# Kernel optimization log

Hardware: AMD Instinct MI355X
Metric: run time of the kernel (lower is better)

Reference implementation:

```python
import jax, jax.numpy as jnp
import numpy as np

B, L, H, V = 16, 512, 256, 32000
HALF = H // 2
EPS_LN = 1e-5
EPS_NORM = 1e-12


def setup_inputs() -> dict:
    key = jax.random.key(0)
    ks = jax.random.split(key, 9)
    s = 0.02
    return {
        "seq": jax.random.randint(ks[0], (B, L), 0, V),
        "embed": jax.random.normal(ks[1], (V, H), jnp.float32) * s,
        "W1": jax.random.normal(ks[2], (2 * H, H), jnp.float32) * s,
        "b1": jnp.zeros((2 * H,), jnp.float32),
        "W2": jax.random.normal(ks[3], (H, 2 * H), jnp.float32) * s,
        "b2": jnp.zeros((H,), jnp.float32),
        "gamma": jnp.ones((H,), jnp.float32),
        "beta": jnp.zeros((H,), jnp.float32),
        "W_sem": jax.random.normal(ks[4], (HALF, H), jnp.float32) * s,
        "W_epi": jax.random.normal(ks[5], (HALF, H), jnp.float32) * s,
        "W_rp": jax.random.normal(ks[6], (H, H), jnp.float32) * s,
        "b_rp": jnp.zeros((H,), jnp.float32),
        "W_out": jax.random.normal(ks[7], (V, H), jnp.float32) * s,
        "b_out": jnp.zeros((V,), jnp.float32),
    }


def _l2norm(x):
    # F.normalize(dim=-1): x / max(||x||, eps)
    n = jnp.sqrt(jnp.sum(x * x, axis=-1, keepdims=True))
    return x / jnp.maximum(n, EPS_NORM)


def reference(seq, embed, W1, b1, W2, b2, gamma, beta, W_sem, W_epi, W_rp, b_rp, W_out, b_out):
    h = embed[seq]                                   # [B, L, H]
    ff = jnp.maximum(h @ W1.T + b1, 0.0) @ W2.T + b2  # MLP with 2H hidden
    x = h + ff
    mu = jnp.mean(x, axis=-1, keepdims=True)
    var = jnp.var(x, axis=-1, keepdims=True)
    h = (x - mu) / jnp.sqrt(var + EPS_LN) * gamma + beta  # LayerNorm

    ks_all = jnp.einsum('blh,kh->blk', h, W_sem)     # [B, L, HALF]
    ke_all = jnp.einsum('blh,kh->blk', h, W_epi)

    def step(carry, kv):
        M_s, M_e = carry
        k_s, k_e = kv                                 # [B, HALF] each
        kns = _l2norm(k_s)
        kne = _l2norm(k_e)
        vps = jnp.einsum('bij,bj->bi', M_s, kns)      # read from fast weights
        vpe = jnp.einsum('bij,bj->bi', M_e, kne)
        M_s = M_s + jnp.einsum('bi,bj->bij', k_s - vps, kns)  # delta-rule write
        M_e = M_e + jnp.einsum('bi,bj->bij', k_e - vpe, kne)
        return (M_s, M_e), None

    M0 = jnp.zeros((B, HALF, HALF), h.dtype)
    # scan over timesteps 0..L-2 (time-major)
    (M_s, M_e), _ = jax.lax.scan(
        step, (M0, M0),
        (jnp.swapaxes(ks_all[:, :-1], 0, 1), jnp.swapaxes(ke_all[:, :-1], 0, 1)))

    cs = jnp.einsum('bij,bj->bi', M_s, ks_all[:, -1])  # read with last-token query
    ce = jnp.einsum('bij,bj->bi', M_e, ke_all[:, -1])
    c = jnp.concatenate([cs, ce], axis=-1)             # [B, H]
    r = c @ W_rp.T + b_rp
    return r @ W_out.T + b_out                          # [B, V]
```

## Files before the change

kernel.cpp:

```cpp
#include <hip/hip_runtime.h>

#define B_ 16
#define L_ 512
#define H_ 256
#define V_ 32000
#define HALF_ 128

typedef __attribute__((ext_vector_type(8))) short short8;
typedef __attribute__((ext_vector_type(4))) float floatx4;

__device__ __forceinline__ unsigned short f2bf(float x) {
  unsigned int u = __float_as_uint(x);
  unsigned int r = (u + 0x7FFFu + ((u >> 16) & 1u)) >> 16;
  return (unsigned short)r;
}

#define BL_(u) __uint_as_float((u) << 16)
#define BH_(u) __uint_as_float((u) & 0xffff0000u)

template <int CTRL>
__device__ __forceinline__ float dpp_xor_add(float x) {
  int y = __builtin_amdgcn_mov_dpp(__float_as_int(x), CTRL, 0xf, 0xf, true);
  return x + __int_as_float(y);
}

__device__ __forceinline__ float redu16(float p) {
  p = dpp_xor_add<0xB1>(p);
  p = dpp_xor_add<0x4E>(p);
  p = dpp_xor_add<0x141>(p);
  p = dpp_xor_add<0x140>(p);
  return p;
}

__global__ __launch_bounds__(256) void prep_kernel(const int* __restrict__ seq,
                                                   const float* __restrict__ embed,
                                                   float* __restrict__ h,
                                                   unsigned short* __restrict__ hbf,
                                                   const float* __restrict__ W1,
                                                   const float* __restrict__ W2,
                                                   const float* __restrict__ Ws,
                                                   const float* __restrict__ We,
                                                   unsigned short* __restrict__ W1b,
                                                   unsigned short* __restrict__ W2b,
                                                   unsigned short* __restrict__ Wcb) {
  int blk = blockIdx.x;
  int tid = threadIdx.x;
  if (blk < 2048) {
    int token = blk * 4 + (tid >> 6);
    int lane = tid & 63;
    int row = seq[token];
    float4 v = ((const float4*)(embed + (size_t)row * H_))[lane];
    ((float4*)(h + (size_t)token * H_))[lane] = v;
    ushort4 o;
    o.x = f2bf(v.x); o.y = f2bf(v.y); o.z = f2bf(v.z); o.w = f2bf(v.w);
    *(ushort4*)(hbf + (size_t)token * H_ + lane * 4) = o;
  } else {
    int i = (blk - 2048) * 256 + tid;
    if (i < 131072) W1b[i] = f2bf(W1[i]);
    else if (i < 262144) W2b[i - 131072] = f2bf(W2[i - 131072]);
    else if (i < 294912) Wcb[i - 262144] = f2bf(Ws[i - 262144]);
    else Wcb[i - 262144] = f2bf(We[i - 294912]);
  }
}

template <int MT, bool RELU, bool BIAS, bool RES, bool OUT_BF16>
__global__ __launch_bounds__(256) void gemm_mfma(const unsigned short* __restrict__ A,
                                                 const unsigned short* __restrict__ Bw,
                                                 const float* __restrict__ bias,
                                                 const float* __restrict__ Res,
                                                 float* __restrict__ Cf,
                                                 unsigned short* __restrict__ Cb,
                                                 int M, int N, int K) {
  constexpr int FI = MT / 32;
  __shared__ unsigned short As[MT * 40];
  __shared__ unsigned short Bs[128 * 40];
  int tid = threadIdx.x;
  int wave = tid >> 6, lane = tid & 63;
  int wm = (wave >> 1) * (MT / 2), wn = (wave & 1) * 64;
  int quad = lane >> 4, l15 = lane & 15;
  int bm = blockIdx.y * MT, bn = blockIdx.x * 128;
  int sr = tid >> 2, sq = tid & 3;

  floatx4 zero = {0.f, 0.f, 0.f, 0.f};
  floatx4 acc[FI][4];
#pragma unroll
  for (int fi = 0; fi < FI; fi++)
#pragma unroll
    for (int fj = 0; fj < 4; fj++) acc[fi][fj] = zero;

  for (int k0 = 0; k0 < K; k0 += 32) {
    uint4 av0 = *(const uint4*)(A + (size_t)(bm + sr) * K + k0 + sq * 8);
    uint4 av1;
    if (MT == 128) av1 = *(const uint4*)(A + (size_t)(bm + 64 + sr) * K + k0 + sq * 8);
    uint4 bv0 = *(const uint4*)(Bw + (size_t)(bn + sr) * K + k0 + sq * 8);
    uint4 bv1 = *(const uint4*)(Bw + (size_t)(bn + 64 + sr) * K + k0 + sq * 8);
    __syncthreads();
    *(uint4*)(As + sr * 40 + sq * 8) = av0;
    if (MT == 128) *(uint4*)(As + (64 + sr) * 40 + sq * 8) = av1;
    *(uint4*)(Bs + sr * 40 + sq * 8) = bv0;
    *(uint4*)(Bs + (64 + sr) * 40 + sq * 8) = bv1;
    __syncthreads();
    short8 af[FI], bf[4];
#pragma unroll
    for (int f = 0; f < FI; f++) af[f] = *(const short8*)(As + (wm + f * 16 + l15) * 40 + quad * 8);
#pragma unroll
    for (int f = 0; f < 4; f++) bf[f] = *(const short8*)(Bs + (wn + f * 16 + l15) * 40 + quad * 8);
#pragma unroll
    for (int fi = 0; fi < FI; fi++)
#pragma unroll
      for (int fj = 0; fj < 4; fj++)
        acc[fi][fj] = __builtin_amdgcn_mfma_f32_16x16x32_bf16(af[fi], bf[fj], acc[fi][fj], 0, 0, 0);
  }

#pragma unroll
  for (int fi = 0; fi < FI; fi++) {
#pragma unroll
    for (int fj = 0; fj < 4; fj++) {
      int col = bn + wn + fj * 16 + l15;
      float bb = BIAS ? bias[col] : 0.f;
#pragma unroll
      for (int rg = 0; rg < 4; rg++) {
        int row = bm + wm + fi * 16 + quad * 4 + rg;
        float v = acc[fi][fj][rg] + bb;
        if (RES) v += Res[(size_t)row * N + col];
        if (RELU) v = fmaxf(v, 0.f);
        if (OUT_BF16) Cb[(size_t)row * N + col] = f2bf(v);
        else Cf[(size_t)row * N + col] = v;
      }
    }
  }
}

__global__ void ln_kernel(const float* __restrict__ x, const float* __restrict__ gamma,
                          const float* __restrict__ beta, unsigned short* __restrict__ yb) {
  int row = blockIdx.x;
  int lane = threadIdx.x;
  float4 v = ((const float4*)(x + (size_t)row * H_))[lane];
  float s = v.x + v.y + v.z + v.w;
  float sq = v.x * v.x + v.y * v.y + v.z * v.z + v.w * v.w;
#pragma unroll
  for (int off = 32; off >= 1; off >>= 1) {
    s += __shfl_xor(s, off);
    sq += __shfl_xor(sq, off);
  }
  float mu = s * (1.f / H_);
  float var = sq * (1.f / H_) - mu * mu;
  float inv = rsqrtf(var + 1e-5f);
  float4 g = ((const float4*)gamma)[lane];
  float4 b = ((const float4*)beta)[lane];
  ushort4 o;
  o.x = f2bf((v.x - mu) * inv * g.x + b.x);
  o.y = f2bf((v.y - mu) * inv * g.y + b.y);
  o.z = f2bf((v.z - mu) * inv * g.z + b.z);
  o.w = f2bf((v.w - mu) * inv * g.w + b.w);
  *(ushort4*)(yb + (size_t)row * H_ + lane * 4) = o;
}

__global__ __launch_bounds__(256) void normalize_kernel(const float* __restrict__ kcat,
                                                        unsigned short* __restrict__ khat) {
  int e = blockIdx.x * 4 + (threadIdx.x >> 6);
  int lane = threadIdx.x & 63;
  int idxm = e >> 9, t = e & 511;
  int b = idxm >> 1, mat = idxm & 1;
  const float* kp = kcat + ((size_t)b * L_ + t) * 256 + mat * 128;
  float2 v = ((const float2*)kp)[lane];
  float s = v.x * v.x + v.y * v.y;
#pragma unroll
  for (int off = 32; off >= 1; off >>= 1) s += __shfl_xor(s, off);
  float inv = 1.f / fmaxf(sqrtf(s), 1e-12f);
  ushort2 o;
  o.x = f2bf(v.x * inv);
  o.y = f2bf(v.y * inv);
  *(ushort2*)(khat + (size_t)e * HALF_ + lane * 2) = o;
}

__global__ __launch_bounds__(256) void gram_kernel(const unsigned short* __restrict__ khat,
                                                   float* __restrict__ gram) {
  int e = blockIdx.x * 4 + (threadIdx.x >> 6);
  int lane = threadIdx.x & 63;
  int idxm = e >> 7, ch = e & 127;
  const unsigned short* kp = khat + ((size_t)idxm * L_ + ch * 4) * HALF_ + lane * 2;
  float2 a[4];
#pragma unroll
  for (int i = 0; i < 4; i++) {
    unsigned int w = *(const unsigned int*)(kp + i * HALF_);
    a[i].x = BL_(w);
    a[i].y = BH_(w);
  }
  float s01 = a[0].x * a[1].x + a[0].y * a[1].y;
  float s02 = a[0].x * a[2].x + a[0].y * a[2].y;
  float s03 = a[0].x * a[3].x + a[0].y * a[3].y;
  float s12 = a[1].x * a[2].x + a[1].y * a[2].y;
  float s13 = a[1].x * a[3].x + a[1].y * a[3].y;
  float s23 = a[2].x * a[3].x + a[2].y * a[3].y;
#pragma unroll
  for (int off = 32; off >= 1; off >>= 1) {
    s01 += __shfl_xor(s01, off);
    s02 += __shfl_xor(s02, off);
    s03 += __shfl_xor(s03, off);
    s12 += __shfl_xor(s12, off);
    s13 += __shfl_xor(s13, off);
    s23 += __shfl_xor(s23, off);
  }
  if (lane == 0) {
    float4 g0 = {s01, s02, s03, s12};
    float2 g1 = {s13, s23};
    *(float4*)(gram + (size_t)e * 8) = g0;
    *(float2*)(gram + (size_t)e * 8 + 4) = g1;
  }
}

#define UNPK(P, K)                                                         \
  float K##0 = BL_(P.x), K##1 = BH_(P.x), K##2 = BL_(P.y), K##3 = BH_(P.y), \
        K##4 = BL_(P.z), K##5 = BH_(P.z), K##6 = BL_(P.w), K##7 = BH_(P.w);

#define DOT8(K, OUT)                                                     \
  float OUT;                                                             \
  {                                                                      \
    float a_ = m[0] * K##0 + m[1] * K##1, b_ = m[2] * K##2 + m[3] * K##3, \
          c_ = m[4] * K##4 + m[5] * K##5, d_ = m[6] * K##6 + m[7] * K##7; \
    OUT = (a_ + b_) + (c_ + d_);                                         \
  }

#define SCAN_STEP(PK, PR)                                                \
  do {                                                                   \
    UNPK(PK, kz)                                                         \
    DOT8(kz, p_)                                                         \
    p_ = redu16(p_);                                                     \
    float sS = PR - p_;                                                  \
    m[0] += sS * kz0; m[1] += sS * kz1; m[2] += sS * kz2; m[3] += sS * kz3; \
    m[4] += sS * kz4; m[5] += sS * kz5; m[6] += sS * kz6; m[7] += sS * kz7; \
  } while (0)

__global__ __launch_bounds__(256) void scan_kernel(const float* __restrict__ kcat,
                                                   const unsigned short* __restrict__ khat,
                                                   const float* __restrict__ gram,
                                                   float* __restrict__ c) {
  int bid = blockIdx.x;
  int idxm = bid & 31;
  int rg = bid >> 5;
  int b = idxm >> 1, mat = idxm & 1;
  const unsigned short* kh = khat + (size_t)idxm * L_ * HALF_;
  const float* kbase = kcat + (size_t)b * L_ * 256 + mat * HALF_;
  const float* gp = gram + (size_t)idxm * 128 * 8;

  int tid = threadIdx.x;
  int seg = tid & 15;
  int rl = tid >> 4;
  int r = rg * 16 + rl;
  int c0 = seg * 8;
  const float* krow = kbase + r;

  float m[8];
#pragma unroll
  for (int g = 0; g < 8; g++) m[g] = 0.f;

  uint4 pk0 = *(const uint4*)(kh + 0 * HALF_ + c0);
  uint4 pk1 = *(const uint4*)(kh + 1 * HALF_ + c0);
  uint4 pk2 = *(const uint4*)(kh + 2 * HALF_ + c0);
  uint4 pk3 = *(const uint4*)(kh + 3 * HALF_ + c0);
  float pr0 = krow[0], pr1 = krow[256], pr2 = krow[512], pr3 = krow[768];
  float4 g03 = *(const float4*)(gp);
  float2 g45 = *(const float2*)(gp + 4);

  for (int ch = 0; ch < 127; ch++) {
    const unsigned short* kn = kh + (size_t)(ch + 1) * 4 * HALF_ + c0;
    uint4 n0 = *(const uint4*)(kn);
    uint4 n1 = *(const uint4*)(kn + HALF_);
    uint4 n2 = *(const uint4*)(kn + 2 * HALF_);
    uint4 n3 = *(const uint4*)(kn + 3 * HALF_);
    const float* rn = krow + (size_t)(ch + 1) * 4 * 256;
    float nr0 = rn[0], nr1 = rn[256], nr2 = rn[512], nr3 = rn[768];
    float4 ng03 = *(const float4*)(gp + (size_t)(ch + 1) * 8);
    float2 ng45 = *(const float2*)(gp + (size_t)(ch + 1) * 8 + 4);

    {
      UNPK(pk0, ka) UNPK(pk1, kb) UNPK(pk2, kc) UNPK(pk3, kd)
      DOT8(ka, p0) DOT8(kb, p1) DOT8(kc, p2) DOT8(kd, p3)
      p0 = redu16(p0);
      p1 = redu16(p1);
      p2 = redu16(p2);
      p3 = redu16(p3);
      float d0 = pr0 - p0;
      float d1 = pr1 - p1 - g03.x * d0;
      float d2 = pr2 - p2 - g03.y * d0 - g03.w * d1;
      float d3 = pr3 - p3 - g03.z * d0 - g45.x * d1 - g45.y * d2;
      m[0] += d0 * ka0 + d1 * kb0 + d2 * kc0 + d3 * kd0;
      m[1] += d0 * ka1 + d1 * kb1 + d2 * kc1 + d3 * kd1;
      m[2] += d0 * ka2 + d1 * kb2 + d2 * kc2 + d3 * kd2;
      m[3] += d0 * ka3 + d1 * kb3 + d2 * kc3 + d3 * kd3;
      m[4] += d0 * ka4 + d1 * kb4 + d2 * kc4 + d3 * kd4;
      m[5] += d0 * ka5 + d1 * kb5 + d2 * kc5 + d3 * kd5;
      m[6] += d0 * ka6 + d1 * kb6 + d2 * kc6 + d3 * kd6;
      m[7] += d0 * ka7 + d1 * kb7 + d2 * kc7 + d3 * kd7;
    }

    pk0 = n0; pk1 = n1; pk2 = n2; pk3 = n3;
    pr0 = nr0; pr1 = nr1; pr2 = nr2; pr3 = nr3;
    g03 = ng03; g45 = ng45;
  }

  SCAN_STEP(pk0, pr0);
  SCAN_STEP(pk1, pr1);
  SCAN_STEP(pk2, pr2);

  float4 qa = *(const float4*)(kbase + (size_t)511 * 256 + c0);
  float4 qb = *(const float4*)(kbase + (size_t)511 * 256 + c0 + 4);
  float pa = m[0] * qa.x + m[1] * qa.y, pb2 = m[2] * qa.z + m[3] * qa.w;
  float pc = m[4] * qb.x + m[5] * qb.y, pd = m[6] * qb.z + m[7] * qb.w;
  float p = redu16((pa + pb2) + (pc + pd));
  if (seg == 0) c[(size_t)b * H_ + mat * HALF_ + r] = p;
}

__global__ void rp_kernel(const float* __restrict__ c, const float* __restrict__ Wrp,
                          const float* __restrict__ brp, float* __restrict__ r) {
  int b = blockIdx.x;
  int n = threadIdx.x;
  __shared__ float cs[H_];
  cs[n] = c[(size_t)b * H_ + n];
  __syncthreads();
  const float4* w4 = (const float4*)(Wrp + (size_t)n * H_);
  const float4* c4 = (const float4*)cs;
  float acc = 0.f;
#pragma unroll 8
  for (int k = 0; k < H_ / 4; k++) {
    float4 w = w4[k], cc = c4[k];
    acc += w.x * cc.x + w.y * cc.y + w.z * cc.z + w.w * cc.w;
  }
  r[(size_t)b * H_ + n] = acc + brp[n];
}

__global__ __launch_bounds__(256) void out_kernel(const float* __restrict__ r,
                                                  const float* __restrict__ Wout,
                                                  const float* __restrict__ bout,
                                                  float* __restrict__ out) {
  __shared__ float rs[16 * 272];
  __shared__ float obuf[16 * 68];
  int tid = threadIdx.x;
#pragma unroll
  for (int q = 0; q < 16; q++) {
    int idx = q * 256 + tid;
    int bb = idx >> 8, cc = idx & 255;
    rs[bb * 272 + cc + 4 * (cc >> 6)] = r[idx];
  }
  __syncthreads();
  int row = tid >> 2, part = tid & 3;
  int v = blockIdx.x * 64 + row;
  const float4* w4 = (const float4*)(Wout + (size_t)v * H_ + part * 64);
  float acc[16];
#pragma unroll
  for (int bb = 0; bb < 16; bb++) acc[bb] = 0.f;
#pragma unroll 4
  for (int j = 0; j < 16; j++) {
    float4 w = w4[j];
#pragma unroll
    for (int bb = 0; bb < 16; bb++) {
      float4 rv = *(const float4*)&rs[bb * 272 + part * 68 + j * 4];
      acc[bb] += w.x * rv.x + w.y * rv.y + w.z * rv.z + w.w * rv.w;
    }
  }
  float bo = bout[v];
#pragma unroll
  for (int bb = 0; bb < 16; bb++) {
    acc[bb] = dpp_xor_add<0xB1>(acc[bb]);
    acc[bb] = dpp_xor_add<0x4E>(acc[bb]);
  }
#pragma unroll
  for (int q = 0; q < 4; q++) {
    int bb = part * 4 + q;
    obuf[bb * 68 + row] = acc[bb] + bo;
  }
  __syncthreads();
#pragma unroll
  for (int q = 0; q < 4; q++) {
    int idx = q * 256 + tid;
    int bb = idx >> 6, vl = idx & 63;
    out[(size_t)bb * V_ + blockIdx.x * 64 + vl] = obuf[bb * 68 + vl];
  }
}

extern "C" void kernel_launch(void* const* d_in, const int* in_sizes, int n_in,
                              void* d_out, int out_size, void* d_ws, size_t ws_size,
                              hipStream_t stream) {
  const int* seq = (const int*)d_in[0];
  const float* embed = (const float*)d_in[1];
  const float* W1 = (const float*)d_in[2];
  const float* b1 = (const float*)d_in[3];
  const float* W2 = (const float*)d_in[4];
  const float* b2 = (const float*)d_in[5];
  const float* gamma = (const float*)d_in[6];
  const float* beta = (const float*)d_in[7];
  const float* Wsem = (const float*)d_in[8];
  const float* Wepi = (const float*)d_in[9];
  const float* Wrp = (const float*)d_in[10];
  const float* brp = (const float*)d_in[11];
  const float* Wout = (const float*)d_in[12];
  const float* bout = (const float*)d_in[13];
  float* out = (float*)d_out;

  float* ws = (float*)d_ws;
  float* h = ws;
  float* x = h;
  float* kcat = ws + 2097152;
  unsigned short* a1b = (unsigned short*)kcat;
  unsigned short* hbf = (unsigned short*)(ws + 4194304);
  float* gram = ws + 4718592;
  unsigned short* hnb = (unsigned short*)(ws + 5242880);
  unsigned short* khat = (unsigned short*)(ws + 6291456);
  unsigned short* W1b = (unsigned short*)(ws + 7340032);
  unsigned short* W2b = (unsigned short*)(ws + 7405568);
  unsigned short* Wcb = (unsigned short*)(ws + 7471104);
  float* c = ws + 7503872;
  float* r = ws + 7508000;

  prep_kernel<<<3328, 256, 0, stream>>>(seq, embed, h, hbf, W1, W2, Wsem, Wepi, W1b, W2b, Wcb);
  gemm_mfma<128, true, true, false, true><<<dim3(4, 64), 256, 0, stream>>>(
      hbf, W1b, b1, nullptr, nullptr, a1b, 8192, 512, 256);
  gemm_mfma<64, false, true, true, false><<<dim3(2, 128), 256, 0, stream>>>(
      a1b, W2b, b2, h, x, nullptr, 8192, 256, 512);
  ln_kernel<<<8192, 64, 0, stream>>>(x, gamma, beta, hnb);
  gemm_mfma<64, false, false, false, false><<<dim3(2, 128), 256, 0, stream>>>(
      hnb, Wcb, nullptr, nullptr, kcat, nullptr, 8192, 256, 256);
  normalize_kernel<<<4096, 256, 0, stream>>>(kcat, khat);
  gram_kernel<<<1024, 256, 0, stream>>>(khat, gram);
  scan_kernel<<<256, 256, 0, stream>>>(kcat, khat, gram, c);
  rp_kernel<<<16, 256, 0, stream>>>(c, Wrp, brp, r);
  out_kernel<<<500, 256, 0, stream>>>(r, Wout, bout, out);
}
```

Before: 271.7 us.

## Fuse key projection with L2 normalization and restructure scan with LDS-staged fp32 keys

Replaces the generic key-projection GEMM, normalize and Gram kernels with one kproj kernel. It computes both key projections per 32-row tile, L2-normalizes them in registers and writes fp32 normalized keys plus a transposed raw-key layout. The scan kernel drops the 4-step blocked Gram correction and instead runs the plain sequential delta rule, streaming normalized keys through double-buffered LDS filled by async global-to-LDS copies. The GEMM also gains register prefetch of the next K-slice, and the workspace layout is compacted. This removes two launches and intermediate round trips, but the scan now has a serial reduction on every step instead of one per four steps.

```diff
diff --git a/kernel.cpp b/kernel.cpp
--- a/kernel.cpp
+++ b/kernel.cpp
@@ -14,9 +14,6 @@
   unsigned int r = (u + 0x7FFFu + ((u >> 16) & 1u)) >> 16;
   return (unsigned short)r;
 }
-
-#define BL_(u) __uint_as_float((u) << 16)
-#define BH_(u) __uint_as_float((u) & 0xffff0000u)
 
 template <int CTRL>
 __device__ __forceinline__ float dpp_xor_add(float x) {
@@ -30,6 +27,12 @@
   p = dpp_xor_add<0x141>(p);
   p = dpp_xor_add<0x140>(p);
   return p;
+}
+
+__device__ __forceinline__ void async_cp16(const float* g, float* l) {
+  __builtin_amdgcn_global_load_lds(
+      (const __attribute__((address_space(1))) void*)g,
+      (__attribute__((address_space(3))) void*)l, 16, 0, 0);
 }
 
 __global__ __launch_bounds__(256) void prep_kernel(const int* __restrict__ seq,
@@ -88,18 +91,25 @@
 #pragma unroll
     for (int fj = 0; fj < 4; fj++) acc[fi][fj] = zero;
 
+  uint4 av0, av1, bv0, bv1;
+  av0 = *(const uint4*)(A + (size_t)(bm + sr) * K + sq * 8);
+  if (MT == 128) av1 = *(const uint4*)(A + (size_t)(bm + 64 + sr) * K + sq * 8);
+  bv0 = *(const uint4*)(Bw + (size_t)(bn + sr) * K + sq * 8);
+  bv1 = *(const uint4*)(Bw + (size_t)(bn + 64 + sr) * K + sq * 8);
+
   for (int k0 = 0; k0 < K; k0 += 32) {
-    uint4 av0 = *(const uint4*)(A + (size_t)(bm + sr) * K + k0 + sq * 8);
-    uint4 av1;
-    if (MT == 128) av1 = *(const uint4*)(A + (size_t)(bm + 64 + sr) * K + k0 + sq * 8);
-    uint4 bv0 = *(const uint4*)(Bw + (size_t)(bn + sr) * K + k0 + sq * 8);
-    uint4 bv1 = *(const uint4*)(Bw + (size_t)(bn + 64 + sr) * K + k0 + sq * 8);
     __syncthreads();
     *(uint4*)(As + sr * 40 + sq * 8) = av0;
     if (MT == 128) *(uint4*)(As + (64 + sr) * 40 + sq * 8) = av1;
     *(uint4*)(Bs + sr * 40 + sq * 8) = bv0;
     *(uint4*)(Bs + (64 + sr) * 40 + sq * 8) = bv1;
     __syncthreads();
+    if (k0 + 32 < K) {
+      av0 = *(const uint4*)(A + (size_t)(bm + sr) * K + k0 + 32 + sq * 8);
+      if (MT == 128) av1 = *(const uint4*)(A + (size_t)(bm + 64 + sr) * K + k0 + 32 + sq * 8);
+      bv0 = *(const uint4*)(Bw + (size_t)(bn + sr) * K + k0 + 32 + sq * 8);
+      bv1 = *(const uint4*)(Bw + (size_t)(bn + 64 + sr) * K + k0 + 32 + sq * 8);
+    }
     short8 af[FI], bf[4];
 #pragma unroll
     for (int f = 0; f < FI; f++) af[f] = *(const short8*)(As + (wm + f * 16 + l15) * 40 + quad * 8);
@@ -156,159 +166,201 @@
   *(ushort4*)(yb + (size_t)row * H_ + lane * 4) = o;
 }
 
-__global__ __launch_bounds__(256) void normalize_kernel(const float* __restrict__ kcat,
-                                                        unsigned short* __restrict__ khat) {
-  int e = blockIdx.x * 4 + (threadIdx.x >> 6);
-  int lane = threadIdx.x & 63;
-  int idxm = e >> 9, t = e & 511;
-  int b = idxm >> 1, mat = idxm & 1;
-  const float* kp = kcat + ((size_t)b * L_ + t) * 256 + mat * 128;
-  float2 v = ((const float2*)kp)[lane];
-  float s = v.x * v.x + v.y * v.y;
-#pragma unroll
-  for (int off = 32; off >= 1; off >>= 1) s += __shfl_xor(s, off);
-  float inv = 1.f / fmaxf(sqrtf(s), 1e-12f);
-  ushort2 o;
-  o.x = f2bf(v.x * inv);
-  o.y = f2bf(v.y * inv);
-  *(ushort2*)(khat + (size_t)e * HALF_ + lane * 2) = o;
-}
-
-__global__ __launch_bounds__(256) void gram_kernel(const unsigned short* __restrict__ khat,
-                                                   float* __restrict__ gram) {
-  int e = blockIdx.x * 4 + (threadIdx.x >> 6);
-  int lane = threadIdx.x & 63;
-  int idxm = e >> 7, ch = e & 127;
-  const unsigned short* kp = khat + ((size_t)idxm * L_ + ch * 4) * HALF_ + lane * 2;
-  float2 a[4];
-#pragma unroll
-  for (int i = 0; i < 4; i++) {
-    unsigned int w = *(const unsigned int*)(kp + i * HALF_);
-    a[i].x = BL_(w);
-    a[i].y = BH_(w);
-  }
-  float s01 = a[0].x * a[1].x + a[0].y * a[1].y;
-  float s02 = a[0].x * a[2].x + a[0].y * a[2].y;
-  float s03 = a[0].x * a[3].x + a[0].y * a[3].y;
-  float s12 = a[1].x * a[2].x + a[1].y * a[2].y;
-  float s13 = a[1].x * a[3].x + a[1].y * a[3].y;
-  float s23 = a[2].x * a[3].x + a[2].y * a[3].y;
-#pragma unroll
-  for (int off = 32; off >= 1; off >>= 1) {
-    s01 += __shfl_xor(s01, off);
-    s02 += __shfl_xor(s02, off);
-    s03 += __shfl_xor(s03, off);
-    s12 += __shfl_xor(s12, off);
-    s13 += __shfl_xor(s13, off);
-    s23 += __shfl_xor(s23, off);
-  }
-  if (lane == 0) {
-    float4 g0 = {s01, s02, s03, s12};
-    float2 g1 = {s13, s23};
-    *(float4*)(gram + (size_t)e * 8) = g0;
-    *(float2*)(gram + (size_t)e * 8 + 4) = g1;
-  }
-}
-
-#define UNPK(P, K)                                                         \
-  float K##0 = BL_(P.x), K##1 = BH_(P.x), K##2 = BL_(P.y), K##3 = BH_(P.y), \
-        K##4 = BL_(P.z), K##5 = BH_(P.z), K##6 = BL_(P.w), K##7 = BH_(P.w);
-
-#define DOT8(K, OUT)                                                     \
-  float OUT;                                                             \
-  {                                                                      \
-    float a_ = m[0] * K##0 + m[1] * K##1, b_ = m[2] * K##2 + m[3] * K##3, \
-          c_ = m[4] * K##4 + m[5] * K##5, d_ = m[6] * K##6 + m[7] * K##7; \
-    OUT = (a_ + b_) + (c_ + d_);                                         \
-  }
-
-#define SCAN_STEP(PK, PR)                                                \
+__global__ __launch_bounds__(256) void kproj_kernel(const unsigned short* __restrict__ hnb,
+                                                    const unsigned short* __restrict__ Wcb,
+                                                    float* __restrict__ khat,
+                                                    float* __restrict__ kT) {
+  __shared__ unsigned short As[32 * 40];
+  __shared__ unsigned short Bs[256 * 40];
+  int tid = threadIdx.x;
+  int wave = tid >> 6, lane = tid & 63;
+  int wm = (wave >> 1) * 16, wnh = wave & 1, wn = wnh * 128;
+  int quad = lane >> 4, l15 = lane & 15;
+  int bm = blockIdx.x * 32;
+
+  floatx4 zero = {0.f, 0.f, 0.f, 0.f};
+  floatx4 acc[8];
+#pragma unroll
+  for (int fj = 0; fj < 8; fj++) acc[fj] = zero;
+
+  int sr = tid >> 2, sq = tid & 3;
+  uint4 av, bv[4];
+  if (tid < 128) av = *(const uint4*)(hnb + (size_t)(bm + sr) * H_ + sq * 8);
+#pragma unroll
+  for (int q = 0; q < 4; q++) {
+    int unit = q * 256 + tid;
+    bv[q] = *(const uint4*)(Wcb + (size_t)(unit >> 2) * H_ + (unit & 3) * 8);
+  }
+
+  for (int k0 = 0; k0 < 256; k0 += 32) {
+    __syncthreads();
+    if (tid < 128) *(uint4*)(As + sr * 40 + sq * 8) = av;
+#pragma unroll
+    for (int q = 0; q < 4; q++) {
+      int unit = q * 256 + tid;
+      *(uint4*)(Bs + (unit >> 2) * 40 + (unit & 3) * 8) = bv[q];
+    }
+    __syncthreads();
+    if (k0 + 32 < 256) {
+      if (tid < 128) av = *(const uint4*)(hnb + (size_t)(bm + sr) * H_ + k0 + 32 + sq * 8);
+#pragma unroll
+      for (int q = 0; q < 4; q++) {
+        int unit = q * 256 + tid;
+        bv[q] = *(const uint4*)(Wcb + (size_t)(unit >> 2) * H_ + k0 + 32 + (unit & 3) * 8);
+      }
+    }
+    short8 af = *(const short8*)(As + (wm + l15) * 40 + quad * 8);
+    short8 bf[8];
+#pragma unroll
+    for (int fj = 0; fj < 8; fj++)
+      bf[fj] = *(const short8*)(Bs + (wn + fj * 16 + l15) * 40 + quad * 8);
+#pragma unroll
+    for (int fj = 0; fj < 8; fj++)
+      acc[fj] = __builtin_amdgcn_mfma_f32_16x16x32_bf16(af, bf[fj], acc[fj], 0, 0, 0);
+  }
+
+  int b = bm >> 9;
+  int idxm = b * 2 + wnh;
+  int tloc0 = (bm & 511) + wm + quad * 4;
+  float inv[4];
+#pragma unroll
+  for (int rg = 0; rg < 4; rg++) {
+    float ssq = 0.f;
+#pragma unroll
+    for (int fj = 0; fj < 8; fj++) ssq += acc[fj][rg] * acc[fj][rg];
+    ssq = redu16(ssq);
+    inv[rg] = 1.f / fmaxf(sqrtf(ssq), 1e-12f);
+  }
+#pragma unroll
+  for (int fj = 0; fj < 8; fj++) {
+    int ch = fj * 16 + l15;
+    int j = ch >> 2, e = ch & 3;
+    int pj = (j & 1) ? (16 + (j >> 1)) : (j >> 1);
+    int pcol = pj * 4 + e;
+#pragma unroll
+    for (int rg = 0; rg < 4; rg++)
+      khat[((size_t)idxm * L_ + tloc0 + rg) * HALF_ + pcol] = acc[fj][rg] * inv[rg];
+    float4 raw = {acc[fj][0], acc[fj][1], acc[fj][2], acc[fj][3]};
+    *(float4*)(kT + (size_t)idxm * (HALF_ * L_) + (size_t)ch * L_ + tloc0) = raw;
+  }
+}
+
+#define STEP(KP, KR)                                                     \
   do {                                                                   \
-    UNPK(PK, kz)                                                         \
-    DOT8(kz, p_)                                                         \
+    float t0_ = m[0] * KP[0] + m[1] * KP[1];                             \
+    float t1_ = m[2] * KP[2] + m[3] * KP[3];                             \
+    float t2_ = m[4] * KP[4] + m[5] * KP[5];                             \
+    float t3_ = m[6] * KP[6] + m[7] * KP[7];                             \
+    float p_ = (t0_ + t1_) + (t2_ + t3_);                                \
     p_ = redu16(p_);                                                     \
-    float sS = PR - p_;                                                  \
-    m[0] += sS * kz0; m[1] += sS * kz1; m[2] += sS * kz2; m[3] += sS * kz3; \
-    m[4] += sS * kz4; m[5] += sS * kz5; m[6] += sS * kz6; m[7] += sS * kz7; \
+    float s_ = (KR) - p_;                                                \
+    m[0] += s_ * KP[0]; m[1] += s_ * KP[1]; m[2] += s_ * KP[2];          \
+    m[3] += s_ * KP[3]; m[4] += s_ * KP[4]; m[5] += s_ * KP[5];          \
+    m[6] += s_ * KP[6]; m[7] += s_ * KP[7];                              \
   } while (0)
 
-__global__ __launch_bounds__(256) void scan_kernel(const float* __restrict__ kcat,
-                                                   const unsigned short* __restrict__ khat,
-                                                   const float* __restrict__ gram,
+__global__ __launch_bounds__(256) void scan_kernel(const float* __restrict__ khat,
+                                                   const float* __restrict__ kT,
                                                    float* __restrict__ c) {
+  __shared__ float sk[2][64 * 128];
   int bid = blockIdx.x;
   int idxm = bid & 31;
   int rg = bid >> 5;
   int b = idxm >> 1, mat = idxm & 1;
-  const unsigned short* kh = khat + (size_t)idxm * L_ * HALF_;
-  const float* kbase = kcat + (size_t)b * L_ * 256 + mat * HALF_;
-  const float* gp = gram + (size_t)idxm * 128 * 8;
+  const float* kh = khat + (size_t)idxm * L_ * HALF_;
+  const float* kTi = kT + (size_t)idxm * HALF_ * L_;
 
   int tid = threadIdx.x;
-  int seg = tid & 15;
-  int rl = tid >> 4;
+  int wave = tid >> 6, lane = tid & 63;
+  int seg = tid & 15, rl = tid >> 4;
   int r = rg * 16 + rl;
   int c0 = seg * 8;
-  const float* krow = kbase + r;
+  const float* krow = kTi + (size_t)r * L_;
 
   float m[8];
 #pragma unroll
   for (int g = 0; g < 8; g++) m[g] = 0.f;
 
-  uint4 pk0 = *(const uint4*)(kh + 0 * HALF_ + c0);
-  uint4 pk1 = *(const uint4*)(kh + 1 * HALF_ + c0);
-  uint4 pk2 = *(const uint4*)(kh + 2 * HALF_ + c0);
-  uint4 pk3 = *(const uint4*)(kh + 3 * HALF_ + c0);
-  float pr0 = krow[0], pr1 = krow[256], pr2 = krow[512], pr3 = krow[768];
-  float4 g03 = *(const float4*)(gp);
-  float2 g45 = *(const float2*)(gp + 4);
-
-  for (int ch = 0; ch < 127; ch++) {
-    const unsigned short* kn = kh + (size_t)(ch + 1) * 4 * HALF_ + c0;
-    uint4 n0 = *(const uint4*)(kn);
-    uint4 n1 = *(const uint4*)(kn + HALF_);
-    uint4 n2 = *(const uint4*)(kn + 2 * HALF_);
-    uint4 n3 = *(const uint4*)(kn + 3 * HALF_);
-    const float* rn = krow + (size_t)(ch + 1) * 4 * 256;
-    float nr0 = rn[0], nr1 = rn[256], nr2 = rn[512], nr3 = rn[768];
-    float4 ng03 = *(const float4*)(gp + (size_t)(ch + 1) * 8);
-    float2 ng45 = *(const float2*)(gp + (size_t)(ch + 1) * 8 + 4);
-
+  {
+    const float* g0 = kh + wave * 2048 + lane * 4;
+    float* l0 = &sk[0][wave * 2048];
+#pragma unroll
+    for (int j = 0; j < 8; j++) async_cp16(g0 + j * 256, l0 + j * 256);
+  }
+  __syncthreads();
+
+  float4 krn = *(const float4*)(krow);
+  const float* lb = &sk[0][0] + seg * 4;
+
+  for (int ch = 0; ch < 7; ch++) {
     {
-      UNPK(pk0, ka) UNPK(pk1, kb) UNPK(pk2, kc) UNPK(pk3, kd)
-      DOT8(ka, p0) DOT8(kb, p1) DOT8(kc, p2) DOT8(kd, p3)
-      p0 = redu16(p0);
-      p1 = redu16(p1);
-      p2 = redu16(p2);
-      p3 = redu16(p3);
-      float d0 = pr0 - p0;
-      float d1 = pr1 - p1 - g03.x * d0;
-      float d2 = pr2 - p2 - g03.y * d0 - g03.w * d1;
-      float d3 = pr3 - p3 - g03.z * d0 - g45.x * d1 - g45.y * d2;
-      m[0] += d0 * ka0 + d1 * kb0 + d2 * kc0 + d3 * kd0;
-      m[1] += d0 * ka1 + d1 * kb1 + d2 * kc1 + d3 * kd1;
-      m[2] += d0 * ka2 + d1 * kb2 + d2 * kc2 + d3 * kd2;
-      m[3] += d0 * ka3 + d1 * kb3 + d2 * kc3 + d3 * kd3;
-      m[4] += d0 * ka4 + d1 * kb4 + d2 * kc4 + d3 * kd4;
-      m[5] += d0 * ka5 + d1 * kb5 + d2 * kc5 + d3 * kd5;
-      m[6] += d0 * ka6 + d1 * kb6 + d2 * kc6 + d3 * kd6;
-      m[7] += d0 * ka7 + d1 * kb7 + d2 * kc7 + d3 * kd7;
-    }
-
-    pk0 = n0; pk1 = n1; pk2 = n2; pk3 = n3;
-    pr0 = nr0; pr1 = nr1; pr2 = nr2; pr3 = nr3;
-    g03 = ng03; g45 = ng45;
-  }
-
-  SCAN_STEP(pk0, pr0);
-  SCAN_STEP(pk1, pr1);
-  SCAN_STEP(pk2, pr2);
-
-  float4 qa = *(const float4*)(kbase + (size_t)511 * 256 + c0);
-  float4 qb = *(const float4*)(kbase + (size_t)511 * 256 + c0 + 4);
-  float pa = m[0] * qa.x + m[1] * qa.y, pb2 = m[2] * qa.z + m[3] * qa.w;
-  float pc = m[4] * qb.x + m[5] * qb.y, pd = m[6] * qb.z + m[7] * qb.w;
-  float p = redu16((pa + pb2) + (pc + pd));
+      const float* gs = kh + (size_t)(ch + 1) * 8192 + wave * 2048 + lane * 4;
+      float* ls = &sk[(ch + 1) & 1][wave * 2048];
+#pragma unroll
+      for (int j = 0; j < 8; j++) async_cp16(gs + j * 256, ls + j * 256);
+    }
+    const float* base = lb + (ch & 1) * 8192;
+    float pk[4][8];
+#pragma unroll
+    for (int u = 0; u < 4; u++) {
+      *(float4*)&pk[u][0] = *(const float4*)(base + u * 128);
+      *(float4*)&pk[u][4] = *(const float4*)(base + u * 128 + 64);
+    }
+    for (int g = 0; g < 15; g++) {
+      float4 krc = krn;
+      krn = *(const float4*)(krow + ch * 64 + g * 4 + 4);
+#pragma unroll
+      for (int u = 0; u < 4; u++) {
+        STEP(pk[u], ((u == 0) ? krc.x : (u == 1) ? krc.y : (u == 2) ? krc.z : krc.w));
+        int tn = g * 4 + u + 4;
+        *(float4*)&pk[u][0] = *(const float4*)(base + tn * 128);
+        *(float4*)&pk[u][4] = *(const float4*)(base + tn * 128 + 64);
+      }
+    }
+    {
+      float4 krc = krn;
+      krn = *(const float4*)(krow + ch * 64 + 64);
+      STEP(pk[0], krc.x);
+      STEP(pk[1], krc.y);
+      STEP(pk[2], krc.z);
+      STEP(pk[3], krc.w);
+    }
+    __syncthreads();
+  }
+
+  {
+    const float* base = lb + 8192;
+    float pk[4][8];
+#pragma unroll
+    for (int u = 0; u < 4; u++) {
+      *(float4*)&pk[u][0] = *(const float4*)(base + u * 128);
+      *(float4*)&pk[u][4] = *(const float4*)(base + u * 128 + 64);
+    }
+    for (int g = 0; g < 15; g++) {
+      float4 krc = krn;
+      krn = *(const float4*)(krow + 448 + g * 4 + 4);
+#pragma unroll
+      for (int u = 0; u < 4; u++) {
+        STEP(pk[u], ((u == 0) ? krc.x : (u == 1) ? krc.y : (u == 2) ? krc.z : krc.w));
+        int tn = g * 4 + u + 4;
+        *(float4*)&pk[u][0] = *(const float4*)(base + tn * 128);
+        *(float4*)&pk[u][4] = *(const float4*)(base + tn * 128 + 64);
+      }
+    }
+    float4 krc = krn;
+    STEP(pk[0], krc.x);
+    STEP(pk[1], krc.y);
+    STEP(pk[2], krc.z);
+  }
+
+  float q[8];
+#pragma unroll
+  for (int j = 0; j < 8; j++) q[j] = kTi[(size_t)(c0 + j) * L_ + 511];
+  float t0 = m[0] * q[0] + m[1] * q[1];
+  float t1 = m[2] * q[2] + m[3] * q[3];
+  float t2 = m[4] * q[4] + m[5] * q[5];
+  float t3 = m[6] * q[6] + m[7] * q[7];
+  float p = redu16((t0 + t1) + (t2 + t3));
   if (seg == 0) c[(size_t)b * H_ + mat * HALF_ + r] = p;
 }
 
@@ -400,30 +452,25 @@
 
   float* ws = (float*)d_ws;
   float* h = ws;
-  float* x = h;
-  float* kcat = ws + 2097152;
-  unsigned short* a1b = (unsigned short*)kcat;
+  float* kT = ws;
+  unsigned short* a1b = (unsigned short*)(ws + 2097152);
+  float* khat = ws + 2097152;
   unsigned short* hbf = (unsigned short*)(ws + 4194304);
-  float* gram = ws + 4718592;
   unsigned short* hnb = (unsigned short*)(ws + 5242880);
-  unsigned short* khat = (unsigned short*)(ws + 6291456);
-  unsigned short* W1b = (unsigned short*)(ws + 7340032);
-  unsigned short* W2b = (unsigned short*)(ws + 7405568);
-  unsigned short* Wcb = (unsigned short*)(ws + 7471104);
-  float* c = ws + 7503872;
-  float* r = ws + 7508000;
+  unsigned short* W1b = (unsigned short*)(ws + 6291456);
+  unsigned short* W2b = (unsigned short*)(ws + 6356992);
+  unsigned short* Wcb = (unsigned short*)(ws + 6422528);
+  float* c = ws + 6455296;
+  float* r = ws + 6459392;
 
   prep_kernel<<<3328, 256, 0, stream>>>(seq, embed, h, hbf, W1, W2, Wsem, Wepi, W1b, W2b, Wcb);
   gemm_mfma<128, true, true, false, true><<<dim3(4, 64), 256, 0, stream>>>(
       hbf, W1b, b1, nullptr, nullptr, a1b, 8192, 512, 256);
   gemm_mfma<64, false, true, true, false><<<dim3(2, 128), 256, 0, stream>>>(
-      a1b, W2b, b2, h, x, nullptr, 8192, 256, 512);
-  ln_kernel<<<8192, 64, 0, stream>>>(x, gamma, beta, hnb);
-  gemm_mfma<64, false, false, false, false><<<dim3(2, 128), 256, 0, stream>>>(
-      hnb, Wcb, nullptr, nullptr, kcat, nullptr, 8192, 256, 256);
-  normalize_kernel<<<4096, 256, 0, stream>>>(kcat, khat);
-  gram_kernel<<<1024, 256, 0, stream>>>(khat, gram);
-  scan_kernel<<<256, 256, 0, stream>>>(kcat, khat, gram, c);
+      a1b, W2b, b2, h, h, nullptr, 8192, 256, 512);
+  ln_kernel<<<8192, 64, 0, stream>>>(h, gamma, beta, hnb);
+  kproj_kernel<<<256, 256, 0, stream>>>(hnb, Wcb, khat, kT);
+  scan_kernel<<<256, 256, 0, stream>>>(khat, kT, c);
   rp_kernel<<<16, 256, 0, stream>>>(c, Wrp, brp, r);
   out_kernel<<<500, 256, 0, stream>>>(r, Wout, bout, out);
 }
```

After: 231.4 us. 14.8% less time.
